# Kernel tuning notes

Measured on AMD Instinct MI355X. Metric: run time of the kernel, lower is better.

## Reference

```python
import jax, jax.numpy as jnp
import numpy as np

V, E, H, L, T, B = 10000, 512, 1024, 2, 128, 64


def setup_inputs() -> dict:
    key = jax.random.key(0)
    ks = jax.random.split(key, 40)
    d = {}
    d["inputs"] = jax.random.randint(ks[0], (T, B), 0, V)
    d["hidden"] = jnp.zeros((L, B, H), jnp.float32)
    d["emb"] = jax.random.uniform(ks[1], (V, E), minval=-0.1, maxval=0.1)
    k = float(1.0 / np.sqrt(H))
    i = 2
    for l in range(L):
        isz = E if l == 0 else H
        for nm, bn in (("Wr", "br"), ("Wz", "bz"), ("Wh", "bh")):
            d[f"{nm}{l}"] = jax.random.uniform(ks[i], (H, isz), minval=-k, maxval=k); i += 1
            d[f"{bn}{l}"] = jax.random.uniform(ks[i], (H,), minval=-k, maxval=k); i += 1
        for nm in ("Ur", "Uz", "Uh"):
            d[f"{nm}{l}"] = jax.random.uniform(ks[i], (H, H), minval=-k, maxval=k); i += 1
    d["Wout"] = jax.random.uniform(ks[i], (V, H), minval=-0.1, maxval=0.1)
    d["bout"] = jnp.zeros((V,), jnp.float32)
    return d


def _gru_cell(x, h, Wr, br, Wz, bz, Wh, bh, Ur, Uz, Uh):
    # dropout is identity (dp_keep_prob=1.0)
    r = jax.nn.sigmoid(x @ Wr.T + br + h @ Ur.T)
    z = jax.nn.sigmoid(x @ Wz.T + bz + h @ Uz.T)
    h_tilde = jnp.tanh(x @ Wh.T + bh + (r * h) @ Uh.T)
    return (1.0 - z) * h + z * h_tilde


def reference(inputs, hidden, emb,
              Wr0, br0, Wz0, bz0, Wh0, bh0, Ur0, Uz0, Uh0,
              Wr1, br1, Wz1, bz1, Wh1, bh1, Ur1, Uz1, Uh1,
              Wout, bout):
    params = [
        (Wr0, br0, Wz0, bz0, Wh0, bh0, Ur0, Uz0, Uh0),
        (Wr1, br1, Wz1, bz1, Wh1, bh1, Ur1, Uz1, Uh1),
    ]
    x_emb = emb[inputs]  # [T, B, E]

    def step(carry, x_t):
        hs = []
        inp = x_t
        for l in range(L):
            h_new = _gru_cell(inp, carry[l], *params[l])
            hs.append(h_new)
            inp = h_new
        return jnp.stack(hs), inp

    h_final, top = jax.lax.scan(step, hidden, x_emb)  # top: [T, B, H]
    logits = top @ Wout.T + bout  # [T, B, V]
    return logits, h_final
```

## Files before the change

kernel.cpp:

```cpp
#include <hip/hip_runtime.h>
#include <hip/hip_bf16.h>
#include <math.h>

#define V 10000
#define E 512
#define H 1024
#define T 128
#define B 64
#define NWG 256
#define LDK 1032

typedef __bf16 bf16x8 __attribute__((ext_vector_type(8)));
typedef float f32x4 __attribute__((ext_vector_type(4)));
typedef unsigned short ushort8 __attribute__((ext_vector_type(8)));

__device__ __forceinline__ void store_f32_sc(float* p, float v) {
    asm volatile("global_store_dword %0, %1, off sc0 sc1" :: "v"(p), "v"(v) : "memory");
}
__device__ __forceinline__ int load_i32_sc(const int* p) {
    int r;
    asm volatile("global_load_dword %0, %1, off sc0 sc1\n\ts_waitcnt vmcnt(0)"
                 : "=v"(r) : "v"(p) : "memory");
    return r;
}

__device__ __forceinline__ void gridbar_grp(int* gcnt, int gen) {
    asm volatile("s_waitcnt vmcnt(0)" ::: "memory");
    __syncthreads();
    if (threadIdx.x == 0)
        __hip_atomic_fetch_add(gcnt + (blockIdx.x & 7) * 32, 1,
                               __ATOMIC_RELAXED, __HIP_MEMORY_SCOPE_AGENT);
    if (threadIdx.x < 8) {
        const int target = gen * 8;
        while (load_i32_sc(gcnt + threadIdx.x * 32) < target)
            __builtin_amdgcn_s_sleep(2);
    }
    __syncthreads();
}

__device__ inline void splitpack(float4 v, uint2& hi, uint2& lo) {
    unsigned u0 = __float_as_uint(v.x), u1 = __float_as_uint(v.y);
    unsigned u2 = __float_as_uint(v.z), u3 = __float_as_uint(v.w);
    hi.x = __builtin_amdgcn_perm(u1, u0, 0x07060302u);
    hi.y = __builtin_amdgcn_perm(u3, u2, 0x07060302u);
    float l0 = v.x - __uint_as_float(u0 & 0xFFFF0000u);
    float l1 = v.y - __uint_as_float(u1 & 0xFFFF0000u);
    float l2 = v.z - __uint_as_float(u2 & 0xFFFF0000u);
    float l3 = v.w - __uint_as_float(u3 & 0xFFFF0000u);
    lo.x = __builtin_amdgcn_perm(__float_as_uint(l1), __float_as_uint(l0), 0x07060302u);
    lo.y = __builtin_amdgcn_perm(__float_as_uint(l3), __float_as_uint(l2), 0x07060302u);
}

__device__ __forceinline__ bf16x8 ld8(const unsigned short* p) {
    return __builtin_bit_cast(bf16x8, *(const ushort8*)p);
}
__device__ __forceinline__ f32x4 mfma3(f32x4 acc, bf16x8 ah, bf16x8 al,
                                       bf16x8 bh, bf16x8 bl) {
    acc = __builtin_amdgcn_mfma_f32_16x16x32_bf16(ah, bh, acc, 0, 0, 0);
    acc = __builtin_amdgcn_mfma_f32_16x16x32_bf16(al, bh, acc, 0, 0, 0);
    acc = __builtin_amdgcn_mfma_f32_16x16x32_bf16(ah, bl, acc, 0, 0, 0);
    return acc;
}

__global__ __launch_bounds__(256) void gemm_mfma_split(
    const float* __restrict__ A, const float* __restrict__ W,
    const float* __restrict__ bias, float* __restrict__ C,
    const int* __restrict__ rowidx,
    int M, int N, int K, int lda, int ldbw, int ldc, int coff)
{
    __shared__ __align__(16) unsigned short Ah[128 * 40];
    __shared__ __align__(16) unsigned short Al[128 * 40];
    __shared__ __align__(16) unsigned short Bh[128 * 40];
    __shared__ __align__(16) unsigned short Bl[128 * 40];

    const int tid  = threadIdx.x;
    const int lane = tid & 63;
    const int wv   = tid >> 6;
    const int wm   = wv & 1, wn = wv >> 1;
    const int bn = blockIdx.x * 128;
    const int bm = blockIdx.y * 128;

    const float* apt[4];
    const float* bpt[4];
    bool bok[4];
    unsigned lofs[4];
    #pragma unroll
    for (int i = 0; i < 4; ++i) {
        int f4 = i * 256 + tid, r = f4 >> 3, kq = f4 & 7;
        int gm = bm + r;
        int ar = rowidx ? rowidx[gm] : gm;
        apt[i] = A + (size_t)ar * lda + kq * 4;
        int gn = bn + r;
        bok[i] = (gn < N);
        bpt[i] = W + (size_t)(bok[i] ? gn : 0) * ldbw + kq * 4;
        lofs[i] = r * 40 + kq * 4;
    }

    f32x4 acc[4][4];
    #pragma unroll
    for (int i = 0; i < 4; ++i)
        #pragma unroll
        for (int j = 0; j < 4; ++j) acc[i][j] = (f32x4){0.f, 0.f, 0.f, 0.f};

    const int la  = lane & 15;
    const int kg8 = (lane >> 4) * 8;

    for (int k0 = 0; k0 < K; k0 += 32) {
        __syncthreads();
        #pragma unroll
        for (int i = 0; i < 4; ++i) {
            float4 va = *(const float4*)(apt[i] + k0);
            uint2 h, l;
            splitpack(va, h, l);
            *(uint2*)&Ah[lofs[i]] = h;
            *(uint2*)&Al[lofs[i]] = l;
            float4 vb = {0.f, 0.f, 0.f, 0.f};
            if (bok[i]) vb = *(const float4*)(bpt[i] + k0);
            splitpack(vb, h, l);
            *(uint2*)&Bh[lofs[i]] = h;
            *(uint2*)&Bl[lofs[i]] = l;
        }
        __syncthreads();

        bf16x8 ah[4], al[4];
        #pragma unroll
        for (int mt = 0; mt < 4; ++mt) {
            int row = (wm * 64 + mt * 16 + la) * 40 + kg8;
            ah[mt] = ld8(&Ah[row]);
            al[mt] = ld8(&Al[row]);
        }
        #pragma unroll
        for (int nt = 0; nt < 4; ++nt) {
            int row = (wn * 64 + nt * 16 + la) * 40 + kg8;
            bf16x8 bh = ld8(&Bh[row]);
            bf16x8 bl = ld8(&Bl[row]);
            #pragma unroll
            for (int mt = 0; mt < 4; ++mt)
                acc[mt][nt] = mfma3(acc[mt][nt], ah[mt], al[mt], bh, bl);
        }
    }

    #pragma unroll
    for (int mt = 0; mt < 4; ++mt) {
        int mrow = bm + wm * 64 + mt * 16 + (lane >> 4) * 4;
        #pragma unroll
        for (int nt = 0; nt < 4; ++nt) {
            int n = bn + wn * 64 + nt * 16 + la;
            if (n < N) {
                float bi = bias ? bias[n] : 0.f;
                #pragma unroll
                for (int r = 0; r < 4; ++r)
                    C[(size_t)(mrow + r) * ldc + n + coff] = acc[mt][nt][r] + bi;
            }
        }
    }
}

__global__ __launch_bounds__(256) void gemm_wx3(
    const float* __restrict__ A,
    const float* __restrict__ W0, const float* __restrict__ W1, const float* __restrict__ W2,
    const float* __restrict__ b0, const float* __restrict__ b1, const float* __restrict__ b2,
    float* __restrict__ C, const int* __restrict__ rowidx,
    int K, int lda)
{
    __shared__ __align__(16) unsigned short Ah[128 * 40];
    __shared__ __align__(16) unsigned short Al[128 * 40];
    __shared__ __align__(16) unsigned short Bh[128 * 40];
    __shared__ __align__(16) unsigned short Bl[128 * 40];

    const int z = blockIdx.z;
    const float* __restrict__ W    = (z == 0) ? W0 : (z == 1) ? W1 : W2;
    const float* __restrict__ bias = (z == 0) ? b0 : (z == 1) ? b1 : b2;
    const int coff = z * H;

    const int tid  = threadIdx.x;
    const int lane = tid & 63;
    const int wv   = tid >> 6;
    const int wm   = wv & 1, wn = wv >> 1;
    const int bn = blockIdx.x * 128;
    const int bm = blockIdx.y * 128;

    const float* apt[4];
    const float* bpt[4];
    unsigned lofs[4];
    #pragma unroll
    for (int i = 0; i < 4; ++i) {
        int f4 = i * 256 + tid, r = f4 >> 3, kq = f4 & 7;
        int gm = bm + r;
        int ar = rowidx ? rowidx[gm] : gm;
        apt[i] = A + (size_t)ar * lda + kq * 4;
        bpt[i] = W + (size_t)(bn + r) * K + kq * 4;
        lofs[i] = r * 40 + kq * 4;
    }

    f32x4 acc[4][4];
    #pragma unroll
    for (int i = 0; i < 4; ++i)
        #pragma unroll
        for (int j = 0; j < 4; ++j) acc[i][j] = (f32x4){0.f, 0.f, 0.f, 0.f};

    const int la  = lane & 15;
    const int kg8 = (lane >> 4) * 8;

    for (int k0 = 0; k0 < K; k0 += 32) {
        __syncthreads();
        #pragma unroll
        for (int i = 0; i < 4; ++i) {
            float4 va = *(const float4*)(apt[i] + k0);
            uint2 h, l;
            splitpack(va, h, l);
            *(uint2*)&Ah[lofs[i]] = h;
            *(uint2*)&Al[lofs[i]] = l;
            float4 vb = *(const float4*)(bpt[i] + k0);
            splitpack(vb, h, l);
            *(uint2*)&Bh[lofs[i]] = h;
            *(uint2*)&Bl[lofs[i]] = l;
        }
        __syncthreads();

        bf16x8 ah[4], al[4];
        #pragma unroll
        for (int mt = 0; mt < 4; ++mt) {
            int row = (wm * 64 + mt * 16 + la) * 40 + kg8;
            ah[mt] = ld8(&Ah[row]);
            al[mt] = ld8(&Al[row]);
        }
        #pragma unroll
        for (int nt = 0; nt < 4; ++nt) {
            int row = (wn * 64 + nt * 16 + la) * 40 + kg8;
            bf16x8 bh = ld8(&Bh[row]);
            bf16x8 bl = ld8(&Bl[row]);
            #pragma unroll
            for (int mt = 0; mt < 4; ++mt)
                acc[mt][nt] = mfma3(acc[mt][nt], ah[mt], al[mt], bh, bl);
        }
    }

    #pragma unroll
    for (int mt = 0; mt < 4; ++mt) {
        int mrow = bm + wm * 64 + mt * 16 + (lane >> 4) * 4;
        #pragma unroll
        for (int nt = 0; nt < 4; ++nt) {
            int n = bn + wn * 64 + nt * 16 + la;
            float bi = bias[n];
            #pragma unroll
            for (int r = 0; r < 4; ++r)
                C[(size_t)(mrow + r) * (3 * H) + n + coff] = acc[mt][nt][r] + bi;
        }
    }
}

__global__ __launch_bounds__(256) void split_mat(
    const float* __restrict__ U, unsigned short* __restrict__ hi,
    unsigned short* __restrict__ lo, int nf4)
{
    int idx = blockIdx.x * 256 + threadIdx.x;
    if (idx >= nf4) return;
    float4 v = ((const float4*)U)[idx];
    uint2 h, l;
    splitpack(v, h, l);
    ((uint2*)hi)[idx] = h;
    ((uint2*)lo)[idx] = l;
}

__global__ __launch_bounds__(1024, 1) void gru_layer(
    const unsigned short* __restrict__ Uhi, const unsigned short* __restrict__ Ulo,
    const float* __restrict__ Wx, const float* __restrict__ hinit,
    float* __restrict__ hRM, float* __restrict__ rhRM,
    float* __restrict__ hfin, int* cnt)
{
    extern __shared__ char smem[];
    unsigned short* hs_hi = (unsigned short*)smem;
    unsigned short* hs_lo = hs_hi + 16 * LDK;
    f32x4* red = (f32x4*)(hs_lo + 16 * LDK);

    const int tid  = threadIdx.x;
    const int lane = tid & 63;
    const int kh   = __builtin_amdgcn_readfirstlane(tid >> 6);
    const int la   = lane & 15;
    const int kg8  = (lane >> 4) * 8;
    const int erow = (lane >> 4) * 4;
    const int trow = tid >> 6;
    const int tq   = tid & 63;

    const int bid = blockIdx.x;
    const int xcd = bid & 7;
    const int sub = bid >> 3;
    const int grp = sub & 3;
    const int m0  = grp * 16;
    const int j0  = (xcd * 8 + (sub >> 2)) * 16;
    int* gcnt = cnt + grp * 8 * 32;

    const size_t HH = (size_t)H * H;
    const unsigned short* Ur_hi = Uhi;
    const unsigned short* Uz_hi = Uhi + HH;
    const unsigned short* Uh_hi = Uhi + 2 * HH;
    const unsigned short* Ur_lo = Ulo;
    const unsigned short* Uz_lo = Ulo + HH;
    const unsigned short* Uh_lo = Ulo + 2 * HH;

    int gen = 0;
    const int rbase = m0 + erow;

    f32x4 zreg = (f32x4){0.f, 0.f, 0.f, 0.f};
    float hvC[4] = {0.f, 0.f, 0.f, 0.f};
    float wrC[4], wzC[4], whC[4];
    float wrN[4], wzN[4], whN[4];
    if (kh == 0) {
        #pragma unroll
        for (int qq = 0; qq < 4; ++qq) {
            hvC[qq] = hinit[(size_t)(rbase + qq) * H + j0 + la];
            const size_t wb = ((size_t)0 * B + rbase + qq) * (3 * H) + j0 + la;
            wrC[qq] = Wx[wb];
            wzC[qq] = Wx[wb + H];
            whC[qq] = Wx[wb + 2 * H];
        }
    }

    for (int t = 0; t < T; ++t) {
        const float* hprev = (t == 0) ? hinit : (hRM + (size_t)(t - 1) * B * H);

        {
            {
                const float* hrp = hprev + (size_t)(m0 + trow) * H;
                #pragma unroll
                for (int i = 0; i < 4; ++i) {
                    const int c = (tq + i * 64) * 4;
                    float4 v = *(const float4*)(hrp + c);
                    uint2 h2, l2;
                    splitpack(v, h2, l2);
                    *(uint2*)&hs_hi[trow * LDK + c] = h2;
                    *(uint2*)&hs_lo[trow * LDK + c] = l2;
                }
            }
            __syncthreads();
            f32x4 a0 = (f32x4){0.f, 0.f, 0.f, 0.f}, a1 = a0;
            const int kb = kh * 64 + kg8;
            #pragma unroll
            for (int ks = 0; ks < 2; ++ks) {
                const int ko = kb + ks * 32;
                const int ar = la * LDK + ko;
                bf16x8 ah = ld8(&hs_hi[ar]);
                bf16x8 al = ld8(&hs_lo[ar]);
                const size_t ub = (size_t)(j0 + la) * H + ko;
                a0 = mfma3(a0, ah, al, ld8(Ur_hi + ub), ld8(Ur_lo + ub));
                a1 = mfma3(a1, ah, al, ld8(Uz_hi + ub), ld8(Uz_lo + ub));
            }
            if (kh) {
                red[((kh - 1) * 2 + 0) * 64 + lane] = a0;
                red[((kh - 1) * 2 + 1) * 64 + lane] = a1;
            }
            __syncthreads();
            if (kh == 0) {
                #pragma unroll
                for (int w = 0; w < 15; ++w) {
                    a0 += red[(w * 2 + 0) * 64 + lane];
                    a1 += red[(w * 2 + 1) * 64 + lane];
                }
                #pragma unroll
                for (int qq = 0; qq < 4; ++qq) {
                    float rg = 1.f / (1.f + __expf(-(a0[qq] + wrC[qq])));
                    zreg[qq] = 1.f / (1.f + __expf(-(a1[qq] + wzC[qq])));
                    store_f32_sc(rhRM + ((size_t)t * B + rbase + qq) * H + j0 + la,
                                 rg * hvC[qq]);
                }
            }
        }
        gridbar_grp(gcnt, ++gen);

        {
            if (kh == 0 && t + 1 < T) {
                #pragma unroll
                for (int qq = 0; qq < 4; ++qq) {
                    const size_t wb = ((size_t)(t + 1) * B + rbase + qq) * (3 * H) + j0 + la;
                    wrN[qq] = Wx[wb];
                    wzN[qq] = Wx[wb + H];
                    whN[qq] = Wx[wb + 2 * H];
                }
            }
            {
                const float* rrp = rhRM + (size_t)t * B * H + (size_t)(m0 + trow) * H;
                #pragma unroll
                for (int i = 0; i < 4; ++i) {
                    const int c = (tq + i * 64) * 4;
                    float4 v = *(const float4*)(rrp + c);
                    uint2 h2, l2;
                    splitpack(v, h2, l2);
                    *(uint2*)&hs_hi[trow * LDK + c] = h2;
                    *(uint2*)&hs_lo[trow * LDK + c] = l2;
                }
            }
            __syncthreads();
            f32x4 a = (f32x4){0.f, 0.f, 0.f, 0.f};
            const int kb = kh * 64 + kg8;
            #pragma unroll
            for (int ks = 0; ks < 2; ++ks) {
                const int ko = kb + ks * 32;
                const int ar = la * LDK + ko;
                const size_t ub = (size_t)(j0 + la) * H + ko;
                a = mfma3(a, ld8(&hs_hi[ar]), ld8(&hs_lo[ar]),
                          ld8(Uh_hi + ub), ld8(Uh_lo + ub));
            }
            if (kh) red[(kh - 1) * 64 + lane] = a;
            __syncthreads();
            if (kh == 0) {
                #pragma unroll
                for (int w = 0; w < 15; ++w) a += red[w * 64 + lane];
                #pragma unroll
                for (int qq = 0; qq < 4; ++qq) {
                    float ht = tanhf(a[qq] + whC[qq]);
                    float hn = (1.f - zreg[qq]) * hvC[qq] + zreg[qq] * ht;
                    store_f32_sc(hRM + ((size_t)t * B + rbase + qq) * H + j0 + la, hn);
                    if (t == T - 1)
                        store_f32_sc(hfin + (size_t)(rbase + qq) * H + j0 + la, hn);
                    hvC[qq] = hn;
                    wrC[qq] = wrN[qq];
                    wzC[qq] = wzN[qq];
                    whC[qq] = whN[qq];
                }
            }
        }
        gridbar_grp(gcnt, ++gen);
    }
}

extern "C" void kernel_launch(void* const* d_in, const int* in_sizes, int n_in,
                              void* d_out, int out_size, void* d_ws, size_t ws_size,
                              hipStream_t stream)
{
    const int*   tok    = (const int*)d_in[0];
    const float* hidden = (const float*)d_in[1];
    const float* emb    = (const float*)d_in[2];
    const float* Wr0 = (const float*)d_in[3],  *br0 = (const float*)d_in[4];
    const float* Wz0 = (const float*)d_in[5],  *bz0 = (const float*)d_in[6];
    const float* Wh0 = (const float*)d_in[7],  *bh0 = (const float*)d_in[8];
    const float* Ur0 = (const float*)d_in[9],  *Uz0 = (const float*)d_in[10], *Uh0 = (const float*)d_in[11];
    const float* Wr1 = (const float*)d_in[12], *br1 = (const float*)d_in[13];
    const float* Wz1 = (const float*)d_in[14], *bz1 = (const float*)d_in[15];
    const float* Wh1 = (const float*)d_in[16], *bh1 = (const float*)d_in[17];
    const float* Ur1 = (const float*)d_in[18], *Uz1 = (const float*)d_in[19], *Uh1 = (const float*)d_in[20];
    const float* Wout = (const float*)d_in[21], *bout = (const float*)d_in[22];
    float* out = (float*)d_out;

    const size_t HH = (size_t)H * H;

    float* ws    = (float*)d_ws;
    float* Wx    = ws;
    float* h0RM  = Wx    + (size_t)T * B * 3 * H;
    float* rh0RM = h0RM  + (size_t)T * B * H;
    float* h1RM  = rh0RM + (size_t)T * B * H;
    float* rh1RM = h1RM  + (size_t)T * B * H;
    unsigned short* U0hi = (unsigned short*)(rh1RM + (size_t)T * B * H);
    unsigned short* U0lo = U0hi + 3 * HH;
    unsigned short* U1hi = U0lo + 3 * HH;
    unsigned short* U1lo = U1hi + 3 * HH;
    int* cnt0 = (int*)(U1lo + 3 * HH);
    int* cnt1 = cnt0 + 4 * 8 * 32;

    static bool attr_set = false;
    if (!attr_set) {
        (void)hipFuncSetAttribute((const void*)gru_layer,
                                  hipFuncAttributeMaxDynamicSharedMemorySize, 96768);
        attr_set = true;
    }

    (void)hipMemsetAsync(cnt0, 0, 2 * 4 * 8 * 32 * sizeof(int), stream);

    const int nHH = (int)(HH / 4);
    split_mat<<<nHH / 256, 256, 0, stream>>>(Ur0, U0hi + 0 * HH, U0lo + 0 * HH, nHH);
    split_mat<<<nHH / 256, 256, 0, stream>>>(Uz0, U0hi + 1 * HH, U0lo + 1 * HH, nHH);
    split_mat<<<nHH / 256, 256, 0, stream>>>(Uh0, U0hi + 2 * HH, U0lo + 2 * HH, nHH);
    split_mat<<<nHH / 256, 256, 0, stream>>>(Ur1, U1hi + 0 * HH, U1lo + 0 * HH, nHH);
    split_mat<<<nHH / 256, 256, 0, stream>>>(Uz1, U1hi + 1 * HH, U1lo + 1 * HH, nHH);
    split_mat<<<nHH / 256, 256, 0, stream>>>(Uh1, U1hi + 2 * HH, U1lo + 2 * HH, nHH);

    gemm_wx3<<<dim3(H / 128, T * B / 128, 3), 256, 0, stream>>>(
        emb, Wr0, Wz0, Wh0, br0, bz0, bh0, Wx, tok, E, E);

    gru_layer<<<NWG, 1024, 96768, stream>>>(U0hi, U0lo, Wx, hidden,
                                            h0RM, rh0RM, out + (size_t)T * B * V, cnt0);

    gemm_wx3<<<dim3(H / 128, T * B / 128, 3), 256, 0, stream>>>(
        h0RM, Wr1, Wz1, Wh1, br1, bz1, bh1, Wx, nullptr, H, H);

    gru_layer<<<NWG, 1024, 96768, stream>>>(U1hi, U1lo, Wx, hidden + (size_t)B * H,
                                            h1RM, rh1RM,
                                            out + (size_t)T * B * V + (size_t)B * H, cnt1);

    gemm_mfma_split<<<dim3((V + 127) / 128, T * B / 128), 256, 0, stream>>>(
        h1RM, Wout, bout, out, nullptr, T * B, V, H, H, H, V, 0);
}
```

Measured before the change: 3.601 ms.

## Store activations and weights pre-split into bf16 hi/lo planes

All weights (U, W, Wout) and the hidden init are split into bf16 hi/lo pairs once by a single batched split kernel instead of six launches. The GRU layers write h and r*h directly as bf16 hi/lo halves, with r*h in a 32-slot ring buffer, so the recurrent step and the downstream GEMMs load pre-split 16-bit data instead of re-splitting fp32 every tile. This halves per-element bytes for staging reads and removes repeated splitpack ALU work, at the cost of an up-front split pass over the weights and more scalar 16-bit global stores in the recurrent loop.

```diff
diff --git a/kernel.cpp b/kernel.cpp
--- a/kernel.cpp
+++ b/kernel.cpp
@@ -9,6 +9,7 @@
 #define B 64
 #define NWG 256
 #define LDK 1032
+#define RHSLOTS 32
 
 typedef __bf16 bf16x8 __attribute__((ext_vector_type(8)));
 typedef float f32x4 __attribute__((ext_vector_type(4)));
@@ -16,6 +17,9 @@
 
 __device__ __forceinline__ void store_f32_sc(float* p, float v) {
     asm volatile("global_store_dword %0, %1, off sc0 sc1" :: "v"(p), "v"(v) : "memory");
+}
+__device__ __forceinline__ void store_u16_sc(unsigned short* p, unsigned v) {
+    asm volatile("global_store_short %0, %1, off sc0 sc1" :: "v"(p), "v"(v) : "memory");
 }
 __device__ __forceinline__ int load_i32_sc(const int* p) {
     int r;
@@ -50,6 +54,12 @@
     lo.x = __builtin_amdgcn_perm(__float_as_uint(l1), __float_as_uint(l0), 0x07060302u);
     lo.y = __builtin_amdgcn_perm(__float_as_uint(l3), __float_as_uint(l2), 0x07060302u);
 }
+__device__ inline void split1(float f, unsigned& hi, unsigned& lo) {
+    unsigned u = __float_as_uint(f);
+    hi = u >> 16;
+    float l = f - __uint_as_float(u & 0xFFFF0000u);
+    lo = __float_as_uint(l) >> 16;
+}
 
 __device__ __forceinline__ bf16x8 ld8(const unsigned short* p) {
     return __builtin_bit_cast(bf16x8, *(const ushort8*)p);
@@ -62,16 +72,42 @@
     return acc;
 }
 
-__global__ __launch_bounds__(256) void gemm_mfma_split(
-    const float* __restrict__ A, const float* __restrict__ W,
-    const float* __restrict__ bias, float* __restrict__ C,
-    const int* __restrict__ rowidx,
-    int M, int N, int K, int lda, int ldbw, int ldc, int coff)
+struct SplitSeg { const float* src; unsigned short* hi; unsigned short* lo; unsigned end; };
+struct SplitTab { SplitSeg s[14]; };
+
+__global__ __launch_bounds__(256) void split_all(SplitTab tab) {
+    unsigned idx = blockIdx.x * 256 + threadIdx.x;
+    unsigned base = 0;
+    #pragma unroll
+    for (int i = 0; i < 14; ++i) {
+        if (idx < tab.s[i].end) {
+            unsigned off = idx - base;
+            float4 v = ((const float4*)tab.s[i].src)[off];
+            uint2 h, l;
+            splitpack(v, h, l);
+            ((uint2*)tab.s[i].hi)[off] = h;
+            ((uint2*)tab.s[i].lo)[off] = l;
+            return;
+        }
+        base = tab.s[i].end;
+    }
+}
+
+__global__ __launch_bounds__(256) void gemm_wx3h(
+    const float* __restrict__ Af32,
+    const unsigned short* __restrict__ Ahi, const unsigned short* __restrict__ Alo,
+    const unsigned short* __restrict__ Whi, const unsigned short* __restrict__ Wlo,
+    const float* __restrict__ b0, const float* __restrict__ b1, const float* __restrict__ b2,
+    float* __restrict__ C, const int* __restrict__ rowidx, int K)
 {
     __shared__ __align__(16) unsigned short Ah[128 * 40];
     __shared__ __align__(16) unsigned short Al[128 * 40];
     __shared__ __align__(16) unsigned short Bh[128 * 40];
     __shared__ __align__(16) unsigned short Bl[128 * 40];
+
+    const int z = blockIdx.z;
+    const float* __restrict__ bias = (z == 0) ? b0 : (z == 1) ? b1 : b2;
+    const size_t zo = (size_t)z * H * K;
 
     const int tid  = threadIdx.x;
     const int lane = tid & 63;
@@ -81,19 +117,16 @@
     const int bm = blockIdx.y * 128;
 
     const float* apt[4];
-    const float* bpt[4];
-    bool bok[4];
-    unsigned lofs[4];
-    #pragma unroll
-    for (int i = 0; i < 4; ++i) {
-        int f4 = i * 256 + tid, r = f4 >> 3, kq = f4 & 7;
-        int gm = bm + r;
-        int ar = rowidx ? rowidx[gm] : gm;
-        apt[i] = A + (size_t)ar * lda + kq * 4;
-        int gn = bn + r;
-        bok[i] = (gn < N);
-        bpt[i] = W + (size_t)(bok[i] ? gn : 0) * ldbw + kq * 4;
-        lofs[i] = r * 40 + kq * 4;
+    unsigned lofs4[4];
+    if (Af32) {
+        #pragma unroll
+        for (int i = 0; i < 4; ++i) {
+            int f4 = i * 256 + tid, r = f4 >> 3, kq = f4 & 7;
+            int gm = bm + r;
+            int ar = rowidx ? rowidx[gm] : gm;
+            apt[i] = Af32 + (size_t)ar * K + kq * 4;
+            lofs4[i] = r * 40 + kq * 4;
+        }
     }
 
     f32x4 acc[4][4];
@@ -107,18 +140,28 @@
 
     for (int k0 = 0; k0 < K; k0 += 32) {
         __syncthreads();
-        #pragma unroll
-        for (int i = 0; i < 4; ++i) {
-            float4 va = *(const float4*)(apt[i] + k0);
-            uint2 h, l;
-            splitpack(va, h, l);
-            *(uint2*)&Ah[lofs[i]] = h;
-            *(uint2*)&Al[lofs[i]] = l;
-            float4 vb = {0.f, 0.f, 0.f, 0.f};
-            if (bok[i]) vb = *(const float4*)(bpt[i] + k0);
-            splitpack(vb, h, l);
-            *(uint2*)&Bh[lofs[i]] = h;
-            *(uint2*)&Bl[lofs[i]] = l;
+        if (Af32) {
+            #pragma unroll
+            for (int i = 0; i < 4; ++i) {
+                float4 va = *(const float4*)(apt[i] + k0);
+                uint2 h, l;
+                splitpack(va, h, l);
+                *(uint2*)&Ah[lofs4[i]] = h;
+                *(uint2*)&Al[lofs4[i]] = l;
+            }
+        } else {
+            #pragma unroll
+            for (int i = 0; i < 2; ++i) {
+                int u8 = i * 256 + tid, r = u8 >> 2, c = (u8 & 3) * 8;
+                *(ushort8*)&Ah[r * 40 + c] = *(const ushort8*)(Ahi + (size_t)(bm + r) * K + k0 + c);
+                *(ushort8*)&Al[r * 40 + c] = *(const ushort8*)(Alo + (size_t)(bm + r) * K + k0 + c);
+            }
+        }
+        #pragma unroll
+        for (int i = 0; i < 2; ++i) {
+            int u8 = i * 256 + tid, r = u8 >> 2, c = (u8 & 3) * 8;
+            *(ushort8*)&Bh[r * 40 + c] = *(const ushort8*)(Whi + zo + (size_t)(bn + r) * K + k0 + c);
+            *(ushort8*)&Bl[r * 40 + c] = *(const ushort8*)(Wlo + zo + (size_t)(bn + r) * K + k0 + c);
         }
         __syncthreads();
 
@@ -146,32 +189,23 @@
         #pragma unroll
         for (int nt = 0; nt < 4; ++nt) {
             int n = bn + wn * 64 + nt * 16 + la;
-            if (n < N) {
-                float bi = bias ? bias[n] : 0.f;
-                #pragma unroll
-                for (int r = 0; r < 4; ++r)
-                    C[(size_t)(mrow + r) * ldc + n + coff] = acc[mt][nt][r] + bi;
-            }
-        }
-    }
-}
-
-__global__ __launch_bounds__(256) void gemm_wx3(
-    const float* __restrict__ A,
-    const float* __restrict__ W0, const float* __restrict__ W1, const float* __restrict__ W2,
-    const float* __restrict__ b0, const float* __restrict__ b1, const float* __restrict__ b2,
-    float* __restrict__ C, const int* __restrict__ rowidx,
-    int K, int lda)
+            float bi = bias[n];
+            #pragma unroll
+            for (int r = 0; r < 4; ++r)
+                C[(size_t)(mrow + r) * (3 * H) + n + z * H] = acc[mt][nt][r] + bi;
+        }
+    }
+}
+
+__global__ __launch_bounds__(256) void gemm_logits(
+    const unsigned short* __restrict__ Ahi, const unsigned short* __restrict__ Alo,
+    const unsigned short* __restrict__ Bhi, const unsigned short* __restrict__ Blo,
+    const float* __restrict__ bias, float* __restrict__ C, int N, int K)
 {
     __shared__ __align__(16) unsigned short Ah[128 * 40];
     __shared__ __align__(16) unsigned short Al[128 * 40];
     __shared__ __align__(16) unsigned short Bh[128 * 40];
     __shared__ __align__(16) unsigned short Bl[128 * 40];
-
-    const int z = blockIdx.z;
-    const float* __restrict__ W    = (z == 0) ? W0 : (z == 1) ? W1 : W2;
-    const float* __restrict__ bias = (z == 0) ? b0 : (z == 1) ? b1 : b2;
-    const int coff = z * H;
 
     const int tid  = threadIdx.x;
     const int lane = tid & 63;
@@ -180,19 +214,6 @@
     const int bn = blockIdx.x * 128;
     const int bm = blockIdx.y * 128;
 
-    const float* apt[4];
-    const float* bpt[4];
-    unsigned lofs[4];
-    #pragma unroll
-    for (int i = 0; i < 4; ++i) {
-        int f4 = i * 256 + tid, r = f4 >> 3, kq = f4 & 7;
-        int gm = bm + r;
-        int ar = rowidx ? rowidx[gm] : gm;
-        apt[i] = A + (size_t)ar * lda + kq * 4;
-        bpt[i] = W + (size_t)(bn + r) * K + kq * 4;
-        lofs[i] = r * 40 + kq * 4;
-    }
-
     f32x4 acc[4][4];
     #pragma unroll
     for (int i = 0; i < 4; ++i)
@@ -205,16 +226,14 @@
     for (int k0 = 0; k0 < K; k0 += 32) {
         __syncthreads();
         #pragma unroll
-        for (int i = 0; i < 4; ++i) {
-            float4 va = *(const float4*)(apt[i] + k0);
-            uint2 h, l;
-            splitpack(va, h, l);
-            *(uint2*)&Ah[lofs[i]] = h;
-            *(uint2*)&Al[lofs[i]] = l;
-            float4 vb = *(const float4*)(bpt[i] + k0);
-            splitpack(vb, h, l);
-            *(uint2*)&Bh[lofs[i]] = h;
-            *(uint2*)&Bl[lofs[i]] = l;
+        for (int i = 0; i < 2; ++i) {
+            int u8 = i * 256 + tid, r = u8 >> 2, c = (u8 & 3) * 8;
+            *(ushort8*)&Ah[r * 40 + c] = *(const ushort8*)(Ahi + (size_t)(bm + r) * K + k0 + c);
+            *(ushort8*)&Al[r * 40 + c] = *(const ushort8*)(Alo + (size_t)(bm + r) * K + k0 + c);
+            int brow = bn + r;
+            int br = (brow < N) ? brow : 0;
+            *(ushort8*)&Bh[r * 40 + c] = *(const ushort8*)(Bhi + (size_t)br * K + k0 + c);
+            *(ushort8*)&Bl[r * 40 + c] = *(const ushort8*)(Blo + (size_t)br * K + k0 + c);
         }
         __syncthreads();
 
@@ -242,31 +261,22 @@
         #pragma unroll
         for (int nt = 0; nt < 4; ++nt) {
             int n = bn + wn * 64 + nt * 16 + la;
-            float bi = bias[n];
-            #pragma unroll
-            for (int r = 0; r < 4; ++r)
-                C[(size_t)(mrow + r) * (3 * H) + n + coff] = acc[mt][nt][r] + bi;
-        }
-    }
-}
-
-__global__ __launch_bounds__(256) void split_mat(
-    const float* __restrict__ U, unsigned short* __restrict__ hi,
-    unsigned short* __restrict__ lo, int nf4)
-{
-    int idx = blockIdx.x * 256 + threadIdx.x;
-    if (idx >= nf4) return;
-    float4 v = ((const float4*)U)[idx];
-    uint2 h, l;
-    splitpack(v, h, l);
-    ((uint2*)hi)[idx] = h;
-    ((uint2*)lo)[idx] = l;
+            if (n < N) {
+                float bi = bias[n];
+                #pragma unroll
+                for (int r = 0; r < 4; ++r)
+                    C[(size_t)(mrow + r) * N + n] = acc[mt][nt][r] + bi;
+            }
+        }
+    }
 }
 
 __global__ __launch_bounds__(1024, 1) void gru_layer(
     const unsigned short* __restrict__ Uhi, const unsigned short* __restrict__ Ulo,
     const float* __restrict__ Wx, const float* __restrict__ hinit,
-    float* __restrict__ hRM, float* __restrict__ rhRM,
+    const unsigned short* __restrict__ hstg_hi, const unsigned short* __restrict__ hstg_lo,
+    unsigned short* __restrict__ h_hi, unsigned short* __restrict__ h_lo,
+    unsigned short* __restrict__ rh_hi, unsigned short* __restrict__ rh_lo,
     float* __restrict__ hfin, int* cnt)
 {
     extern __shared__ char smem[];
@@ -280,8 +290,6 @@
     const int la   = lane & 15;
     const int kg8  = (lane >> 4) * 8;
     const int erow = (lane >> 4) * 4;
-    const int trow = tid >> 6;
-    const int tq   = tid & 63;
 
     const int bid = blockIdx.x;
     const int xcd = bid & 7;
@@ -318,20 +326,17 @@
     }
 
     for (int t = 0; t < T; ++t) {
-        const float* hprev = (t == 0) ? hinit : (hRM + (size_t)(t - 1) * B * H);
+        const size_t rbs = (size_t)(t & (RHSLOTS - 1)) * B * H;
 
         {
-            {
-                const float* hrp = hprev + (size_t)(m0 + trow) * H;
-                #pragma unroll
-                for (int i = 0; i < 4; ++i) {
-                    const int c = (tq + i * 64) * 4;
-                    float4 v = *(const float4*)(hrp + c);
-                    uint2 h2, l2;
-                    splitpack(v, h2, l2);
-                    *(uint2*)&hs_hi[trow * LDK + c] = h2;
-                    *(uint2*)&hs_lo[trow * LDK + c] = l2;
-                }
+            const unsigned short* ph = (t == 0) ? hstg_hi : (h_hi + (size_t)(t - 1) * B * H);
+            const unsigned short* pl = (t == 0) ? hstg_lo : (h_lo + (size_t)(t - 1) * B * H);
+            #pragma unroll
+            for (int j = 0; j < 2; ++j) {
+                int u8 = j * 1024 + tid;
+                int r = u8 >> 7, c = (u8 & 127) * 8;
+                *(ushort8*)&hs_hi[r * LDK + c] = *(const ushort8*)(ph + (size_t)(m0 + r) * H + c);
+                *(ushort8*)&hs_lo[r * LDK + c] = *(const ushort8*)(pl + (size_t)(m0 + r) * H + c);
             }
             __syncthreads();
             f32x4 a0 = (f32x4){0.f, 0.f, 0.f, 0.f}, a1 = a0;
@@ -361,8 +366,12 @@
                 for (int qq = 0; qq < 4; ++qq) {
                     float rg = 1.f / (1.f + __expf(-(a0[qq] + wrC[qq])));
                     zreg[qq] = 1.f / (1.f + __expf(-(a1[qq] + wzC[qq])));
-                    store_f32_sc(rhRM + ((size_t)t * B + rbase + qq) * H + j0 + la,
-                                 rg * hvC[qq]);
+                    float rh = rg * hvC[qq];
+                    unsigned rhh, rhl;
+                    split1(rh, rhh, rhl);
+                    const size_t ix = rbs + (size_t)(rbase + qq) * H + j0 + la;
+                    store_u16_sc(rh_hi + ix, rhh);
+                    store_u16_sc(rh_lo + ix, rhl);
                 }
             }
         }
@@ -378,17 +387,12 @@
                     whN[qq] = Wx[wb + 2 * H];
                 }
             }
-            {
-                const float* rrp = rhRM + (size_t)t * B * H + (size_t)(m0 + trow) * H;
-                #pragma unroll
-                for (int i = 0; i < 4; ++i) {
-                    const int c = (tq + i * 64) * 4;
-                    float4 v = *(const float4*)(rrp + c);
-                    uint2 h2, l2;
-                    splitpack(v, h2, l2);
-                    *(uint2*)&hs_hi[trow * LDK + c] = h2;
-                    *(uint2*)&hs_lo[trow * LDK + c] = l2;
-                }
+            #pragma unroll
+            for (int j = 0; j < 2; ++j) {
+                int u8 = j * 1024 + tid;
+                int r = u8 >> 7, c = (u8 & 127) * 8;
+                *(ushort8*)&hs_hi[r * LDK + c] = *(const ushort8*)(rh_hi + rbs + (size_t)(m0 + r) * H + c);
+                *(ushort8*)&hs_lo[r * LDK + c] = *(const ushort8*)(rh_lo + rbs + (size_t)(m0 + r) * H + c);
             }
             __syncthreads();
             f32x4 a = (f32x4){0.f, 0.f, 0.f, 0.f};
@@ -410,7 +414,11 @@
                 for (int qq = 0; qq < 4; ++qq) {
                     float ht = tanhf(a[qq] + whC[qq]);
                     float hn = (1.f - zreg[qq]) * hvC[qq] + zreg[qq] * ht;
-                    store_f32_sc(hRM + ((size_t)t * B + rbase + qq) * H + j0 + la, hn);
+                    unsigned hh, hl;
+                    split1(hn, hh, hl);
+                    const size_t ix = (size_t)t * B * H + (size_t)(rbase + qq) * H + j0 + la;
+                    store_u16_sc(h_hi + ix, hh);
+                    store_u16_sc(h_lo + ix, hl);
                     if (t == T - 1)
                         store_f32_sc(hfin + (size_t)(rbase + qq) * H + j0 + la, hn);
                     hvC[qq] = hn;
@@ -443,18 +451,34 @@
     float* out = (float*)d_out;
 
     const size_t HH = (size_t)H * H;
-
-    float* ws    = (float*)d_ws;
-    float* Wx    = ws;
-    float* h0RM  = Wx    + (size_t)T * B * 3 * H;
-    float* rh0RM = h0RM  + (size_t)T * B * H;
-    float* h1RM  = rh0RM + (size_t)T * B * H;
-    float* rh1RM = h1RM  + (size_t)T * B * H;
-    unsigned short* U0hi = (unsigned short*)(rh1RM + (size_t)T * B * H);
-    unsigned short* U0lo = U0hi + 3 * HH;
-    unsigned short* U1hi = U0lo + 3 * HH;
-    unsigned short* U1lo = U1hi + 3 * HH;
-    int* cnt0 = (int*)(U1lo + 3 * HH);
+    const size_t HE = (size_t)H * E;
+    const size_t TBH = (size_t)T * B * H;
+    const size_t VH = (size_t)V * H;
+
+    float* ws = (float*)d_ws;
+    float* Wx = ws;
+    unsigned short* u16 = (unsigned short*)(Wx + 3 * TBH);
+    unsigned short* U0hi = u16;            u16 += 3 * HH;
+    unsigned short* U0lo = u16;            u16 += 3 * HH;
+    unsigned short* U1hi = u16;            u16 += 3 * HH;
+    unsigned short* U1lo = u16;            u16 += 3 * HH;
+    unsigned short* W1hi = u16;            u16 += 3 * HH;
+    unsigned short* W1lo = u16;            u16 += 3 * HH;
+    unsigned short* W0hi = u16;            u16 += 3 * HE;
+    unsigned short* W0lo = u16;            u16 += 3 * HE;
+    unsigned short* Wouthi = u16;          u16 += VH;
+    unsigned short* Woutlo = u16;          u16 += VH;
+    unsigned short* hidhi = u16;           u16 += 2 * (size_t)B * H;
+    unsigned short* hidlo = u16;           u16 += 2 * (size_t)B * H;
+    unsigned short* h0hi = u16;            u16 += TBH;
+    unsigned short* h0lo = u16;            u16 += TBH;
+    unsigned short* h1hi = u16;            u16 += TBH;
+    unsigned short* h1lo = u16;            u16 += TBH;
+    unsigned short* rh0hi = u16;           u16 += (size_t)RHSLOTS * B * H;
+    unsigned short* rh0lo = u16;           u16 += (size_t)RHSLOTS * B * H;
+    unsigned short* rh1hi = u16;           u16 += (size_t)RHSLOTS * B * H;
+    unsigned short* rh1lo = u16;           u16 += (size_t)RHSLOTS * B * H;
+    int* cnt0 = (int*)u16;
     int* cnt1 = cnt0 + 4 * 8 * 32;
 
     static bool attr_set = false;
@@ -466,27 +490,39 @@
 
     (void)hipMemsetAsync(cnt0, 0, 2 * 4 * 8 * 32 * sizeof(int), stream);
 
-    const int nHH = (int)(HH / 4);
-    split_mat<<<nHH / 256, 256, 0, stream>>>(Ur0, U0hi + 0 * HH, U0lo + 0 * HH, nHH);
-    split_mat<<<nHH / 256, 256, 0, stream>>>(Uz0, U0hi + 1 * HH, U0lo + 1 * HH, nHH);
-    split_mat<<<nHH / 256, 256, 0, stream>>>(Uh0, U0hi + 2 * HH, U0lo + 2 * HH, nHH);
-    split_mat<<<nHH / 256, 256, 0, stream>>>(Ur1, U1hi + 0 * HH, U1lo + 0 * HH, nHH);
-    split_mat<<<nHH / 256, 256, 0, stream>>>(Uz1, U1hi + 1 * HH, U1lo + 1 * HH, nHH);
-    split_mat<<<nHH / 256, 256, 0, stream>>>(Uh1, U1hi + 2 * HH, U1lo + 2 * HH, nHH);
-
-    gemm_wx3<<<dim3(H / 128, T * B / 128, 3), 256, 0, stream>>>(
-        emb, Wr0, Wz0, Wh0, br0, bz0, bh0, Wx, tok, E, E);
-
-    gru_layer<<<NWG, 1024, 96768, stream>>>(U0hi, U0lo, Wx, hidden,
-                                            h0RM, rh0RM, out + (size_t)T * B * V, cnt0);
-
-    gemm_wx3<<<dim3(H / 128, T * B / 128, 3), 256, 0, stream>>>(
-        h0RM, Wr1, Wz1, Wh1, br1, bz1, bh1, Wx, nullptr, H, H);
-
-    gru_layer<<<NWG, 1024, 96768, stream>>>(U1hi, U1lo, Wx, hidden + (size_t)B * H,
-                                            h1RM, rh1RM,
-                                            out + (size_t)T * B * V + (size_t)B * H, cnt1);
-
-    gemm_mfma_split<<<dim3((V + 127) / 128, T * B / 128), 256, 0, stream>>>(
-        h1RM, Wout, bout, out, nullptr, T * B, V, H, H, H, V, 0);
-}
+    const unsigned nU = (unsigned)(HH / 4), nW0 = (unsigned)(HE / 4);
+    const unsigned nWout = (unsigned)(VH / 4), nHid = (unsigned)(2 * B * H / 4);
+    SplitTab tab;
+    unsigned acc = 0;
+    const float* srcs[14] = {Ur0, Uz0, Uh0, Ur1, Uz1, Uh1, Wr1, Wz1, Wh1,
+                             Wr0, Wz0, Wh0, Wout, hidden};
+    unsigned short* his[14] = {U0hi, U0hi + HH, U0hi + 2 * HH, U1hi, U1hi + HH, U1hi + 2 * HH,
+                               W1hi, W1hi + HH, W1hi + 2 * HH,
+                               W0hi, W0hi + HE, W0hi + 2 * HE, Wouthi, hidhi};
+    unsigned short* los[14] = {U0lo, U0lo + HH, U0lo + 2 * HH, U1lo, U1lo + HH, U1lo + 2 * HH,
+                               W1lo, W1lo + HH, W1lo + 2 * HH,
+                               W0lo, W0lo + HE, W0lo + 2 * HE, Woutlo, hidlo};
+    unsigned cnts[14] = {nU, nU, nU, nU, nU, nU, nU, nU, nU, nW0, nW0, nW0, nWout, nHid};
+    for (int i = 0; i < 14; ++i) {
+        acc += cnts[i];
+        tab.s[i] = {srcs[i], his[i], los[i], acc};
+    }
+    split_all<<<acc / 256, 256, 0, stream>>>(tab);
+
+    gemm_wx3h<<<dim3(H / 128, T * B / 128, 3), 256, 0, stream>>>(
+        emb, nullptr, nullptr, W0hi, W0lo, br0, bz0, bh0, Wx, tok, E);
+
+    gru_layer<<<NWG, 1024, 96768, stream>>>(
+        U0hi, U0lo, Wx, hidden, hidhi, hidlo,
+        h0hi, h0lo, rh0hi, rh0lo, out + (size_t)T * B * V, cnt0);
+
+    gemm_wx3h<<<dim3(H / 128, T * B / 128, 3), 256, 0, stream>>>(
+        nullptr, h0hi, h0lo, W1hi, W1lo, br1, bz1, bh1, Wx, nullptr, H);
+
+    gru_layer<<<NWG, 1024, 96768, stream>>>(
+        U1hi, U1lo, Wx, hidden + (size_t)B * H, hidhi + (size_t)B * H, hidlo + (size_t)B * H,
+        h1hi, h1lo, rh1hi, rh1lo, out + (size_t)T * B * V + (size_t)B * H, cnt1);
+
+    gemm_logits<<<dim3((V + 127) / 128, T * B / 128), 256, 0, stream>>>(
+        h1hi, h1lo, Wouthi, Woutlo, bout, out, V, H);
+}
```

Measured after the change: 3.723 ms. 3.4% more time.
